# Performance work log

Measured on AMD Instinct MI355X. Metric: run time of the kernel, lower is better.

Reference implementation:

```python
import jax, jax.numpy as jnp
import numpy as np

EPS = 1e-8  # matches F.cosine_similarity default eps


def setup_inputs() -> dict:
    key = jax.random.key(0)
    k1, k2 = jax.random.split(key)
    labels = jax.random.uniform(k1, (8192, 2), dtype=jnp.float32)  # argmax -> random 0/1
    datas = jax.random.normal(k2, (8192, 4096), dtype=jnp.float32)
    return {"labels": labels, "datas": datas}


def reference(labels, datas):
    # labels: [B, C] one-hot (C=2); datas: [B, D]
    lab = jnp.argmax(labels, axis=1)
    mask0 = (lab == 0).astype(datas.dtype)  # normal vectors
    mask1 = (lab == 1).astype(datas.dtype)  # except vectors
    n0 = jnp.sum(mask0)
    n1 = jnp.sum(mask1)

    # mean of label-0 rows (fixed-shape masked mean instead of boolean gather)
    mean_vec = jnp.sum(datas * mask0[:, None], axis=0) / jnp.maximum(n0, 1.0)  # [D]

    # batched cosine similarity of every row vs mean_vec (replaces per-row loop)
    x_norm = jnp.maximum(jnp.linalg.norm(datas, axis=1), EPS)  # [B]
    m_norm = jnp.maximum(jnp.linalg.norm(mean_vec), EPS)       # scalar
    cos = (datas @ mean_vec) / (x_norm * m_norm)               # [B]
    abs_cos = jnp.abs(cos)

    sim_loss = jnp.sum(mask0 * (1.0 - abs_cos)) / jnp.maximum(n0, 1.0)
    differ_loss = jnp.sum(mask1 * abs_cos) / jnp.maximum(n1, 1.0)

    # edge cases: no normals -> both 0; normals but no excepts -> differ 0
    sim_loss = jnp.where(n0 > 0, sim_loss, 0.0)
    differ_loss = jnp.where((n0 > 0) & (n1 > 0), differ_loss, 0.0)
    total_loss = sim_loss + differ_loss
    return (total_loss, sim_loss, differ_loss)
```

## Files before the change

### kernel.cpp

```cpp
#include <hip/hip_runtime.h>
#include <math.h>

#define NROWS 8192
#define NCOLS 4096
#define EPS 1e-8f

__device__ float g_mask[NROWS];
__device__ float g_S[NCOLS];
__device__ float g_partials[256 * NCOLS];
__device__ float g_abs[NROWS];
__device__ float g_scalars[4];

__global__ __launch_bounds__(1024) void k_mask(const float* __restrict__ labels) {
    int t = threadIdx.x;
    int cnt = 0;
    #pragma unroll
    for (int j = 0; j < 8; ++j) {
        int r = t + j * 1024;
        float l0 = labels[2 * r];
        float l1 = labels[2 * r + 1];
        bool m0 = (l0 >= l1);
        g_mask[r] = m0 ? 1.f : 0.f;
        cnt += m0 ? 1 : 0;
    }
    for (int off = 32; off; off >>= 1) cnt += __shfl_xor(cnt, off);
    __shared__ int sh[16];
    int lane = t & 63, w = t >> 6;
    if (lane == 0) sh[w] = cnt;
    __syncthreads();
    if (t == 0) {
        int tot = 0;
        #pragma unroll
        for (int i = 0; i < 16; ++i) tot += sh[i];
        g_scalars[0] = (float)tot;
        g_scalars[1] = (float)(NROWS - tot);
        g_scalars[2] = 0.f;
    }
}

__global__ __launch_bounds__(1024) void k_colsum(const float* __restrict__ datas) {
    int b = blockIdx.x, t = threadIdx.x;
    const float4* d4 = (const float4*)datas;
    float4 acc = {0.f, 0.f, 0.f, 0.f};
    int r0 = b * 32;
    #pragma unroll 4
    for (int r = 0; r < 32; ++r) {
        float m = g_mask[r0 + r];
        float4 v = d4[(size_t)(r0 + r) * (NCOLS / 4) + t];
        acc.x += m * v.x; acc.y += m * v.y; acc.z += m * v.z; acc.w += m * v.w;
    }
    ((float4*)g_partials)[(size_t)b * (NCOLS / 4) + t] = acc;
}

__global__ __launch_bounds__(1024) void k_reduceS() {
    int t = threadIdx.x;
    int cl = t & 255;
    int sub = t >> 8;
    int c = blockIdx.x * 256 + cl;
    float s = 0.f;
    #pragma unroll 8
    for (int j = 0; j < 64; ++j)
        s += g_partials[(size_t)(sub * 64 + j) * NCOLS + c];
    __shared__ float sh[1024];
    sh[t] = s;
    __syncthreads();
    __shared__ float sh2[256];
    if (t < 256) {
        float tot = sh[t] + sh[t + 256] + sh[t + 512] + sh[t + 768];
        g_S[blockIdx.x * 256 + t] = tot;
        sh2[t] = tot * tot;
    }
    __syncthreads();
    if (t == 0) {
        float m = 0.f;
        #pragma unroll
        for (int i = 0; i < 256; ++i) m += sh2[i];
        atomicAdd(&g_scalars[2], m);
    }
}

__global__ __launch_bounds__(256) void k_cos(const float* __restrict__ datas) {
    int t = threadIdx.x;
    int lane = t & 63;
    int wv = (blockIdx.x << 2) + (t >> 6);
    const float4* d4 = (const float4*)datas;
    const float4* s4 = (const float4*)g_S;
    float n0 = g_scalars[0];
    float n0d = fmaxf(n0, 1.f);
    float msq = g_scalars[2];
    float mnorm = fmaxf(sqrtf(msq) / n0d, EPS);
    #pragma unroll
    for (int rr = 0; rr < 2; ++rr) {
        int r = wv + rr * 4096;
        size_t base = (size_t)r * (NCOLS / 4);
        float dot = 0.f, sq = 0.f;
        #pragma unroll 8
        for (int k = 0; k < 16; ++k) {
            float4 v = d4[base + lane + (k << 6)];
            float4 w = s4[lane + (k << 6)];
            dot += v.x * w.x + v.y * w.y + v.z * w.z + v.w * w.w;
            sq  += v.x * v.x + v.y * v.y + v.z * v.z + v.w * v.w;
        }
        for (int off = 32; off; off >>= 1) {
            dot += __shfl_xor(dot, off);
            sq  += __shfl_xor(sq, off);
        }
        if (lane == 0) {
            float xn = fmaxf(sqrtf(sq), EPS);
            float cosv = (dot / n0d) / (xn * mnorm);
            g_abs[r] = fabsf(cosv);
        }
    }
}

__global__ __launch_bounds__(1024) void k_final(float* __restrict__ out) {
    int t = threadIdx.x;
    float sim = 0.f, dif = 0.f;
    #pragma unroll
    for (int j = 0; j < 8; ++j) {
        int r = t + j * 1024;
        float m = g_mask[r];
        float a = g_abs[r];
        sim += m * (1.f - a);
        dif += (1.f - m) * a;
    }
    for (int off = 32; off; off >>= 1) {
        sim += __shfl_xor(sim, off);
        dif += __shfl_xor(dif, off);
    }
    __shared__ float sh[32];
    int lane = t & 63, w = t >> 6;
    if (lane == 0) { sh[w] = sim; sh[w + 16] = dif; }
    __syncthreads();
    if (t == 0) {
        float s = 0.f, d = 0.f;
        #pragma unroll
        for (int i = 0; i < 16; ++i) { s += sh[i]; d += sh[i + 16]; }
        float n0 = g_scalars[0], n1 = g_scalars[1];
        float simL = (n0 > 0.f) ? s / fmaxf(n0, 1.f) : 0.f;
        float difL = (n0 > 0.f && n1 > 0.f) ? d / fmaxf(n1, 1.f) : 0.f;
        out[0] = simL + difL;
        out[1] = simL;
        out[2] = difL;
    }
}

extern "C" void kernel_launch(void* const* d_in, const int* in_sizes, int n_in,
                              void* d_out, int out_size, void* d_ws, size_t ws_size,
                              hipStream_t stream) {
    const float* labels = (const float*)d_in[0];
    const float* datas  = (const float*)d_in[1];
    float* out = (float*)d_out;

    k_mask<<<1, 1024, 0, stream>>>(labels);
    k_colsum<<<256, 1024, 0, stream>>>(datas);
    k_reduceS<<<16, 1024, 0, stream>>>();
    k_cos<<<1024, 256, 0, stream>>>(datas);
    k_final<<<1, 1024, 0, stream>>>(out);
}
```

Measured before the change: 225.6 us.

## Fuse all stages into one cooperative kernel with grid syncs

Replaces the five separate launches (mask, column sum, reduce, cosine, final) with a single cooperative kernel of 256 blocks, using grid.sync between phases. Each block computes its own mask slice, skips loads for label-1 rows in the column sum, and does the cosine pass on the same 32 rows it summed, so those rows may still be in cache. The cosine normalisation by n0 and the mean norm is pulled out algebraically and applied once at the end, which removes the g_abs and g_mask round trips. The cost is three grid-wide barriers, a cooperative launch that needs all 256 blocks resident at once, and per-lane branching on the mask.

```diff
diff --git a/kernel.cpp b/kernel.cpp
--- a/kernel.cpp
+++ b/kernel.cpp
@@ -1,147 +1,147 @@
 #include <hip/hip_runtime.h>
+#include <hip/hip_cooperative_groups.h>
 #include <math.h>
+
+namespace cg = cooperative_groups;
 
 #define NROWS 8192
 #define NCOLS 4096
+#define NB 256
+#define RPB 32
 #define EPS 1e-8f
 
-__device__ float g_mask[NROWS];
+__device__ float g_partials[NB * NCOLS];
 __device__ float g_S[NCOLS];
-__device__ float g_partials[256 * NCOLS];
-__device__ float g_abs[NROWS];
-__device__ float g_scalars[4];
+__device__ float g_n0[NB];
+__device__ float g_msq[NB];
+__device__ float g_A[NB];
+__device__ float g_B[NB];
 
-__global__ __launch_bounds__(1024) void k_mask(const float* __restrict__ labels) {
-    int t = threadIdx.x;
-    int cnt = 0;
-    #pragma unroll
-    for (int j = 0; j < 8; ++j) {
-        int r = t + j * 1024;
-        float l0 = labels[2 * r];
-        float l1 = labels[2 * r + 1];
-        bool m0 = (l0 >= l1);
-        g_mask[r] = m0 ? 1.f : 0.f;
-        cnt += m0 ? 1 : 0;
+__global__ __launch_bounds__(1024, 4) void fused(const float* __restrict__ labels,
+                                                 const float* __restrict__ datas,
+                                                 float* __restrict__ out) {
+    cg::grid_group grid = cg::this_grid();
+    const int b = blockIdx.x, t = threadIdx.x;
+    const int r0 = b * RPB;
+    const float4* d4 = (const float4*)datas;
+
+    __shared__ float sh_mask[RPB];
+    __shared__ float sh2[64][17];
+    __shared__ float sh_red[32];
+
+    if (t < RPB) {
+        float l0 = labels[2 * (r0 + t)];
+        float l1 = labels[2 * (r0 + t) + 1];
+        sh_mask[t] = (l0 >= l1) ? 1.f : 0.f;
     }
-    for (int off = 32; off; off >>= 1) cnt += __shfl_xor(cnt, off);
-    __shared__ int sh[16];
-    int lane = t & 63, w = t >> 6;
-    if (lane == 0) sh[w] = cnt;
     __syncthreads();
     if (t == 0) {
-        int tot = 0;
+        float c = 0.f;
         #pragma unroll
-        for (int i = 0; i < 16; ++i) tot += sh[i];
-        g_scalars[0] = (float)tot;
-        g_scalars[1] = (float)(NROWS - tot);
-        g_scalars[2] = 0.f;
+        for (int r = 0; r < RPB; ++r) c += sh_mask[r];
+        g_n0[b] = c;
     }
-}
 
-__global__ __launch_bounds__(1024) void k_colsum(const float* __restrict__ datas) {
-    int b = blockIdx.x, t = threadIdx.x;
-    const float4* d4 = (const float4*)datas;
     float4 acc = {0.f, 0.f, 0.f, 0.f};
-    int r0 = b * 32;
-    #pragma unroll 4
-    for (int r = 0; r < 32; ++r) {
-        float m = g_mask[r0 + r];
-        float4 v = d4[(size_t)(r0 + r) * (NCOLS / 4) + t];
-        acc.x += m * v.x; acc.y += m * v.y; acc.z += m * v.z; acc.w += m * v.w;
+    for (int r = 0; r < RPB; ++r) {
+        if (sh_mask[r] != 0.f) {
+            float4 v = d4[(size_t)(r0 + r) * (NCOLS / 4) + t];
+            acc.x += v.x; acc.y += v.y; acc.z += v.z; acc.w += v.w;
+        }
     }
     ((float4*)g_partials)[(size_t)b * (NCOLS / 4) + t] = acc;
-}
 
-__global__ __launch_bounds__(1024) void k_reduceS() {
-    int t = threadIdx.x;
-    int cl = t & 255;
-    int sub = t >> 8;
-    int c = blockIdx.x * 256 + cl;
-    float s = 0.f;
-    #pragma unroll 8
-    for (int j = 0; j < 64; ++j)
-        s += g_partials[(size_t)(sub * 64 + j) * NCOLS + c];
-    __shared__ float sh[1024];
-    sh[t] = s;
+    grid.sync();
+
+    {
+        int col = t & 15, row = t >> 4;
+        int c0 = b * 16;
+        float s = 0.f;
+        #pragma unroll
+        for (int j = 0; j < 4; ++j)
+            s += g_partials[(size_t)(row + 64 * j) * NCOLS + c0 + col];
+        sh2[row][col] = s;
+    }
     __syncthreads();
-    __shared__ float sh2[256];
-    if (t < 256) {
-        float tot = sh[t] + sh[t + 256] + sh[t + 512] + sh[t + 768];
-        g_S[blockIdx.x * 256 + t] = tot;
-        sh2[t] = tot * tot;
+    if (t < 16) {
+        float tot = 0.f;
+        #pragma unroll
+        for (int r = 0; r < 64; ++r) tot += sh2[r][t];
+        g_S[b * 16 + t] = tot;
+        sh_red[t] = tot * tot;
     }
     __syncthreads();
     if (t == 0) {
         float m = 0.f;
         #pragma unroll
-        for (int i = 0; i < 256; ++i) m += sh2[i];
-        atomicAdd(&g_scalars[2], m);
+        for (int i = 0; i < 16; ++i) m += sh_red[i];
+        g_msq[b] = m;
     }
-}
 
-__global__ __launch_bounds__(256) void k_cos(const float* __restrict__ datas) {
-    int t = threadIdx.x;
-    int lane = t & 63;
-    int wv = (blockIdx.x << 2) + (t >> 6);
-    const float4* d4 = (const float4*)datas;
-    const float4* s4 = (const float4*)g_S;
-    float n0 = g_scalars[0];
-    float n0d = fmaxf(n0, 1.f);
-    float msq = g_scalars[2];
-    float mnorm = fmaxf(sqrtf(msq) / n0d, EPS);
-    #pragma unroll
-    for (int rr = 0; rr < 2; ++rr) {
-        int r = wv + rr * 4096;
-        size_t base = (size_t)r * (NCOLS / 4);
-        float dot = 0.f, sq = 0.f;
-        #pragma unroll 8
-        for (int k = 0; k < 16; ++k) {
-            float4 v = d4[base + lane + (k << 6)];
-            float4 w = s4[lane + (k << 6)];
-            dot += v.x * w.x + v.y * w.y + v.z * w.z + v.w * w.w;
-            sq  += v.x * v.x + v.y * v.y + v.z * v.z + v.w * v.w;
+    grid.sync();
+
+    {
+        int lane = t & 63, w = t >> 6;
+        const float4* s4 = (const float4*)g_S;
+        float pa = 0.f, pb = 0.f;
+        #pragma unroll
+        for (int rr = 0; rr < 2; ++rr) {
+            int rloc = w * 2 + rr;
+            size_t base = (size_t)(r0 + rloc) * (NCOLS / 4);
+            float dot = 0.f, sq = 0.f;
+            #pragma unroll 4
+            for (int k = 0; k < 16; ++k) {
+                float4 v  = d4[base + lane + (k << 6)];
+                float4 sv = s4[lane + (k << 6)];
+                dot += v.x * sv.x + v.y * sv.y + v.z * sv.z + v.w * sv.w;
+                sq  += v.x * v.x + v.y * v.y + v.z * v.z + v.w * v.w;
+            }
+            #pragma unroll
+            for (int off = 32; off; off >>= 1) {
+                dot += __shfl_xor(dot, off);
+                sq  += __shfl_xor(sq, off);
+            }
+            float a = fabsf(dot) / fmaxf(sqrtf(sq), EPS);
+            float m = sh_mask[rloc];
+            pa += m * a;
+            pb += (1.f - m) * a;
         }
-        for (int off = 32; off; off >>= 1) {
-            dot += __shfl_xor(dot, off);
-            sq  += __shfl_xor(sq, off);
-        }
-        if (lane == 0) {
-            float xn = fmaxf(sqrtf(sq), EPS);
-            float cosv = (dot / n0d) / (xn * mnorm);
-            g_abs[r] = fabsf(cosv);
-        }
+        if (lane == 0) { sh_red[w] = pa; sh_red[w + 16] = pb; }
     }
-}
-
-__global__ __launch_bounds__(1024) void k_final(float* __restrict__ out) {
-    int t = threadIdx.x;
-    float sim = 0.f, dif = 0.f;
-    #pragma unroll
-    for (int j = 0; j < 8; ++j) {
-        int r = t + j * 1024;
-        float m = g_mask[r];
-        float a = g_abs[r];
-        sim += m * (1.f - a);
-        dif += (1.f - m) * a;
-    }
-    for (int off = 32; off; off >>= 1) {
-        sim += __shfl_xor(sim, off);
-        dif += __shfl_xor(dif, off);
-    }
-    __shared__ float sh[32];
-    int lane = t & 63, w = t >> 6;
-    if (lane == 0) { sh[w] = sim; sh[w + 16] = dif; }
     __syncthreads();
     if (t == 0) {
-        float s = 0.f, d = 0.f;
+        float A = 0.f, B = 0.f;
         #pragma unroll
-        for (int i = 0; i < 16; ++i) { s += sh[i]; d += sh[i + 16]; }
-        float n0 = g_scalars[0], n1 = g_scalars[1];
-        float simL = (n0 > 0.f) ? s / fmaxf(n0, 1.f) : 0.f;
-        float difL = (n0 > 0.f && n1 > 0.f) ? d / fmaxf(n1, 1.f) : 0.f;
-        out[0] = simL + difL;
-        out[1] = simL;
-        out[2] = difL;
+        for (int i = 0; i < 16; ++i) { A += sh_red[i]; B += sh_red[i + 16]; }
+        g_A[b] = A; g_B[b] = B;
+    }
+
+    grid.sync();
+
+    if (b == 0 && t < 64) {
+        float n0 = 0.f, msq = 0.f, A = 0.f, B = 0.f;
+        #pragma unroll
+        for (int j = 0; j < 4; ++j) {
+            int i = t + j * 64;
+            n0 += g_n0[i]; msq += g_msq[i]; A += g_A[i]; B += g_B[i];
+        }
+        #pragma unroll
+        for (int off = 32; off; off >>= 1) {
+            n0  += __shfl_xor(n0, off);
+            msq += __shfl_xor(msq, off);
+            A   += __shfl_xor(A, off);
+            B   += __shfl_xor(B, off);
+        }
+        if (t == 0) {
+            float n1 = (float)NROWS - n0;
+            float n0d = fmaxf(n0, 1.f), n1d = fmaxf(n1, 1.f);
+            float D = fmaxf(sqrtf(msq), n0d * EPS);
+            float simL = (n0 > 0.f) ? (n0 - A / D) / n0d : 0.f;
+            float difL = (n0 > 0.f && n1 > 0.f) ? (B / D) / n1d : 0.f;
+            out[0] = simL + difL;
+            out[1] = simL;
+            out[2] = difL;
+        }
     }
 }
 
@@ -151,10 +151,7 @@
     const float* labels = (const float*)d_in[0];
     const float* datas  = (const float*)d_in[1];
     float* out = (float*)d_out;
-
-    k_mask<<<1, 1024, 0, stream>>>(labels);
-    k_colsum<<<256, 1024, 0, stream>>>(datas);
-    k_reduceS<<<16, 1024, 0, stream>>>();
-    k_cos<<<1024, 256, 0, stream>>>(datas);
-    k_final<<<1, 1024, 0, stream>>>(out);
+    void* args[] = {(void*)&labels, (void*)&datas, (void*)&out};
+    hipLaunchCooperativeKernel((const void*)fused, dim3(NB), dim3(1024),
+                               args, 0, stream);
 }
```

After: 312.0 us. 1.38x slower.
